# Kernel tuning notes

Measured on AMD Instinct MI355X. Metric: run time of the kernel, lower is better.

## Reference

```python
import jax, jax.numpy as jnp
import numpy as np

RESERVOIR_SIZE = 2048
EMBED = 768
N_FRAMES = 256
NUM_CLASSES = 1000
BATCH = 128
SPARSITY = 0.05
SPECTRAL_RADIUS = 0.8


def _init_reservoir(key):
    k1, k2 = jax.random.split(key)
    w = jax.random.normal(k1, (RESERVOIR_SIZE, RESERVOIR_SIZE), dtype=jnp.float32)
    mask = (jax.random.uniform(k2, (RESERVOIR_SIZE, RESERVOIR_SIZE)) < SPARSITY).astype(jnp.float32)
    r = w * mask
    # rescale so spectral radius == SPECTRAL_RADIUS (matches torch eigvals-based init)
    eig = np.linalg.eigvals(np.asarray(r))
    max_abs = np.abs(eig).max()
    return r * (SPECTRAL_RADIUS / jnp.float32(max_abs))


def setup_inputs() -> dict:
    key = jax.random.key(0)
    kx, kr, kin, kout = jax.random.split(key, 4)
    x = jax.random.normal(kx, (BATCH, N_FRAMES, EMBED), dtype=jnp.float32)
    reservoir = _init_reservoir(kr)
    W_in = jax.random.normal(kin, (RESERVOIR_SIZE, EMBED), dtype=jnp.float32) * 0.1
    W_out = jax.random.normal(kout, (NUM_CLASSES, RESERVOIR_SIZE), dtype=jnp.float32) * 0.02
    b_out = jnp.zeros((NUM_CLASSES,), dtype=jnp.float32)
    return {"x": x, "reservoir": reservoir, "W_in": W_in, "W_out": W_out, "b_out": b_out}


def reference(x, reservoir, W_in, W_out, b_out):
    # x: [B, T, E]. Precompute input projections for all frames in one GEMM:
    # u[t] = x[:, t] @ W_in.T  -> [T, B, R]
    u = jnp.einsum("bte,re->tbr", x, W_in)
    state0 = jnp.zeros((x.shape[0], reservoir.shape[0]), dtype=x.dtype)

    def step(state, u_t):
        new_state = jnp.tanh(state @ reservoir.T + u_t)
        return new_state, None

    state, _ = jax.lax.scan(step, state0, u)
    # linear head (dropout is identity in eval mode)
    logits = state @ W_out.T + b_out
    return logits
```

## Files before the change

### kernel.cpp

```cpp
#include <hip/hip_runtime.h>
#include <stdint.h>
#include <stddef.h>

#define BATCH 128
#define NFRAMES 256
#define EMBED 768
#define RES 2048
#define NCLS 1000
#define NWG 256

typedef __attribute__((ext_vector_type(8))) short bf16x8;
typedef __attribute__((ext_vector_type(4))) float f32x4;
typedef unsigned short u16;

__device__ inline u16 f2bf(float f) {
    union { float f; unsigned u; } v; v.f = f;
    unsigned r = v.u + 0x7FFFu + ((v.u >> 16) & 1u);
    return (u16)(r >> 16);
}
__device__ inline float bf2f(u16 h) {
    union { unsigned u; float f; } v; v.u = ((unsigned)h) << 16;
    return v.f;
}
__device__ inline float tanh_fast(float x) {
    float z = __builtin_amdgcn_exp2f(x * 2.885390081777927f);
    return 1.f - 2.f * __builtin_amdgcn_rcpf(z + 1.f);
}

__global__ __launch_bounds__(256) void cvt_kernel(const float* __restrict__ in,
                                                  u16* __restrict__ out, int n4) {
    int i = blockIdx.x * blockDim.x + threadIdx.x;
    int stride = gridDim.x * blockDim.x;
    for (; i < n4; i += stride) {
        float4 v = ((const float4*)in)[i];
        ushort4 o;
        o.x = f2bf(v.x); o.y = f2bf(v.y); o.z = f2bf(v.z); o.w = f2bf(v.w);
        ((ushort4*)out)[i] = o;
    }
}

__global__ __launch_bounds__(256) void proj_kernel(const u16* __restrict__ xb,
                                                   const u16* __restrict__ win,
                                                   u16* __restrict__ u) {
    int lane = threadIdx.x & 63;
    int w = threadIdx.x >> 6;
    int wm = w >> 1, wn = w & 1;
    int m0 = blockIdx.x * 128 + wm * 64;
    int n0 = blockIdx.y * 128 + wn * 64;
    int lr = lane & 15;
    int lk = (lane >> 4) * 8;

    f32x4 acc[4][4];
#pragma unroll
    for (int i = 0; i < 4; i++)
#pragma unroll
        for (int j = 0; j < 4; j++) acc[i][j] = (f32x4)0.f;

    for (int kk = 0; kk < EMBED; kk += 32) {
        bf16x8 a[4], b[4];
#pragma unroll
        for (int i = 0; i < 4; i++)
            a[i] = *(const bf16x8*)(xb + (size_t)(m0 + i * 16 + lr) * EMBED + kk + lk);
#pragma unroll
        for (int j = 0; j < 4; j++)
            b[j] = *(const bf16x8*)(win + (size_t)(n0 + j * 16 + lr) * EMBED + kk + lk);
#pragma unroll
        for (int i = 0; i < 4; i++)
#pragma unroll
            for (int j = 0; j < 4; j++)
                acc[i][j] = __builtin_amdgcn_mfma_f32_16x16x32_bf16(a[i], b[j], acc[i][j], 0, 0, 0);
    }

    int rowbase = (lane >> 4) * 4;
#pragma unroll
    for (int i = 0; i < 4; i++) {
#pragma unroll
        for (int j = 0; j < 4; j++) {
#pragma unroll
            for (int q = 0; q < 4; q++) {
                int m = m0 + i * 16 + rowbase + q;
                int n = n0 + j * 16 + lr;
                int bb = m >> 8, tt = m & 255;
                u[((size_t)tt * BATCH + bb) * RES + n] = f2bf(acc[i][j][q]);
            }
        }
    }
}

__global__ __launch_bounds__(512, 1) void recur_kernel(const u16* __restrict__ res,
                                                       u16* __restrict__ u,
                                                       const u16* __restrict__ s0,
                                                       unsigned* __restrict__ flags) {
    __shared__ float part[8][16][66];
    const int lane = threadIdx.x & 63;
    const int w = threadIdx.x >> 6;
    const int rowgrp = (int)(blockIdx.x & 7);
    const int colblk = (int)(blockIdx.x >> 3);
    const int m0 = rowgrp * 16;
    const int n0 = colblk * 64;
    const int lr = lane & 15;
    const int lk = (lane >> 4) * 8;
    const int rb = (lane >> 4) * 4;
    const int kbase = w * 256;
    unsigned* myflag = flags + rowgrp * 32 + colblk;
    const unsigned* pollflag = flags + rowgrp * 32 + (lane & 31);

    bf16x8 bfr[4][8];
#pragma unroll
    for (int jf = 0; jf < 4; jf++)
#pragma unroll
        for (int kk = 0; kk < 8; kk++) {
            const u16* bp = res + (size_t)(n0 + jf * 16 + lr) * RES + kbase + kk * 32 + lk;
            asm volatile("global_load_dwordx4 %0, %1, off"
                         : "=v"(bfr[jf][kk]) : "v"(bp));
        }
    asm volatile("s_waitcnt vmcnt(0)" ::: "memory");

    const int er = threadIdx.x >> 5;
    const int ec = (threadIdx.x & 31) * 2;
    const size_t gidx = (size_t)(m0 + er) * RES + n0 + ec;

    for (int t = 0; t < NFRAMES; t++) {
        const u16* sin = (t == 0) ? s0 : u + (size_t)(t - 1) * BATCH * RES;
        u16* sout = u + (size_t)t * BATCH * RES;
        const u16* abase = sin + (size_t)(m0 + lr) * RES + kbase + lk;

        unsigned uv = *(const unsigned*)(sout + gidx);

        bf16x8 a[8];
#pragma unroll
        for (int kk = 0; kk < 8; kk++)
            asm volatile("global_load_dwordx4 %0, %1, off"
                         : "=v"(a[kk]) : "v"(abase + kk * 32));

        f32x4 acc[4];
#pragma unroll
        for (int jf = 0; jf < 4; jf++) acc[jf] = (f32x4)0.f;

        asm volatile("s_waitcnt vmcnt(4)" ::: "memory");
        __builtin_amdgcn_sched_barrier(0);
#pragma unroll
        for (int kk = 0; kk < 4; kk++)
#pragma unroll
            for (int jf = 0; jf < 4; jf++)
                acc[jf] = __builtin_amdgcn_mfma_f32_16x16x32_bf16(a[kk], bfr[jf][kk], acc[jf], 0, 0, 0);
        asm volatile("s_waitcnt vmcnt(0)" ::: "memory");
        __builtin_amdgcn_sched_barrier(0);
#pragma unroll
        for (int kk = 4; kk < 8; kk++)
#pragma unroll
            for (int jf = 0; jf < 4; jf++)
                acc[jf] = __builtin_amdgcn_mfma_f32_16x16x32_bf16(a[kk], bfr[jf][kk], acc[jf], 0, 0, 0);

#pragma unroll
        for (int jf = 0; jf < 4; jf++)
#pragma unroll
            for (int q = 0; q < 4; q++)
                part[w][rb + q][jf * 16 + lr] = acc[jf][q];
        __syncthreads();

        float sx = 0.f, sy = 0.f;
#pragma unroll
        for (int ww = 0; ww < 8; ww++) {
            float2 v = *(const float2*)&part[ww][er][ec];
            sx += v.x; sy += v.y;
        }
        float v0 = tanh_fast(sx + bf2f((u16)(uv & 0xFFFF)));
        float v1 = tanh_fast(sy + bf2f((u16)(uv >> 16)));
        unsigned pk = (unsigned)f2bf(v0) | ((unsigned)f2bf(v1) << 16);
        asm volatile("global_store_dword %0, %1, off sc0 sc1"
                     :: "v"(sout + gidx), "v"(pk) : "memory");

        asm volatile("s_waitcnt vmcnt(0)" ::: "memory");
        __syncthreads();
        if (t != NFRAMES - 1) {
            unsigned stamp = (unsigned)(t + 1);
            if (w == 0) {
                if (lane == 0)
                    asm volatile("global_store_dword %0, %1, off sc0 sc1"
                                 :: "v"(myflag), "v"(stamp) : "memory");
                unsigned f;
                do {
                    asm volatile("global_load_dword %0, %1, off sc0 sc1\n\ts_waitcnt vmcnt(0)"
                                 : "=v"(f) : "v"(pollflag) : "memory");
                    if (__all((int)(f >= stamp))) break;
                    __builtin_amdgcn_s_sleep(2);
                } while (1);
            }
            __syncthreads();
        }
    }
}

__global__ __launch_bounds__(512) void head_kernel(const u16* __restrict__ sin,
                                                   const u16* __restrict__ wout,
                                                   const float* __restrict__ bias,
                                                   float* __restrict__ out) {
    __shared__ float part[8][32][33];
    int lane = threadIdx.x & 63;
    int w = threadIdx.x >> 6;
    int m0 = blockIdx.x * 32;
    int n0 = blockIdx.y * 32;
    int k0 = w * 256;
    int lr = lane & 15;
    int lk = (lane >> 4) * 8;

    f32x4 acc[2][2];
#pragma unroll
    for (int i = 0; i < 2; i++)
#pragma unroll
        for (int j = 0; j < 2; j++) acc[i][j] = (f32x4)0.f;

    for (int kk = k0; kk < k0 + 256; kk += 32) {
        bf16x8 a[2], b[2];
#pragma unroll
        for (int i = 0; i < 2; i++)
            a[i] = *(const bf16x8*)(sin + (size_t)(m0 + i * 16 + lr) * RES + kk + lk);
#pragma unroll
        for (int j = 0; j < 2; j++) {
            int row = n0 + j * 16 + lr;
            if (row > NCLS - 1) row = NCLS - 1;
            b[j] = *(const bf16x8*)(wout + (size_t)row * RES + kk + lk);
        }
#pragma unroll
        for (int i = 0; i < 2; i++)
#pragma unroll
            for (int j = 0; j < 2; j++)
                acc[i][j] = __builtin_amdgcn_mfma_f32_16x16x32_bf16(a[i], b[j], acc[i][j], 0, 0, 0);
    }

    int rowbase = (lane >> 4) * 4;
#pragma unroll
    for (int i = 0; i < 2; i++)
#pragma unroll
        for (int j = 0; j < 2; j++)
#pragma unroll
            for (int q = 0; q < 4; q++)
                part[w][i * 16 + rowbase + q][j * 16 + lr] = acc[i][j][q];

    __syncthreads();

    for (int idx = threadIdx.x; idx < 1024; idx += 512) {
        int r = idx >> 5, c = idx & 31;
        float s = 0.f;
#pragma unroll
        for (int ww = 0; ww < 8; ww++) s += part[ww][r][c];
        int cg = n0 + c;
        if (cg < NCLS)
            out[(size_t)(m0 + r) * NCLS + cg] = s + bias[cg];
    }
}

extern "C" void kernel_launch(void* const* d_in, const int* in_sizes, int n_in,
                              void* d_out, int out_size, void* d_ws, size_t ws_size,
                              hipStream_t stream) {
    const float* x_f    = (const float*)d_in[0];
    const float* res_f  = (const float*)d_in[1];
    const float* win_f  = (const float*)d_in[2];
    const float* wout_f = (const float*)d_in[3];
    const float* bias   = (const float*)d_in[4];
    float* out = (float*)d_out;

    char* ws = (char*)d_ws;
    size_t off = 0;
    auto alloc = [&](size_t bytes) -> void* {
        void* p = ws + off;
        off += (bytes + 255) & ~(size_t)255;
        return p;
    };
    u16* res_b  = (u16*)alloc((size_t)RES * RES * 2);
    u16* win_b  = (u16*)alloc((size_t)RES * EMBED * 2);
    u16* wout_b = (u16*)alloc((size_t)NCLS * RES * 2);
    u16* x_b    = (u16*)alloc((size_t)BATCH * NFRAMES * EMBED * 2);
    u16* u      = (u16*)alloc((size_t)NFRAMES * BATCH * RES * 2);
    u16* s0     = (u16*)alloc((size_t)BATCH * RES * 2);
    unsigned* flags = (unsigned*)alloc(1024);

    cvt_kernel<<<dim3(1024), dim3(256), 0, stream>>>(res_f, res_b, RES * RES / 4);
    cvt_kernel<<<dim3(512), dim3(256), 0, stream>>>(win_f, win_b, RES * EMBED / 4);
    cvt_kernel<<<dim3(512), dim3(256), 0, stream>>>(wout_f, wout_b, NCLS * RES / 4);
    cvt_kernel<<<dim3(2048), dim3(256), 0, stream>>>(x_f, x_b, BATCH * NFRAMES * EMBED / 4);

    hipMemsetAsync(s0, 0, (size_t)BATCH * RES * 2, stream);
    hipMemsetAsync(flags, 0, 1024, stream);

    proj_kernel<<<dim3(256, 16), dim3(256), 0, stream>>>(x_b, win_b, u);

    void* args[] = { (void*)&res_b, (void*)&u, (void*)&s0, (void*)&flags };
    hipLaunchCooperativeKernel((const void*)recur_kernel, dim3(NWG), dim3(512),
                               args, 0, stream);

    const u16* sfin = u + (size_t)(NFRAMES - 1) * BATCH * RES;
    head_kernel<<<dim3(4, 32), dim3(512), 0, stream>>>(sfin, wout_b, bias, out);
}
```

Measured before the change: 1.405 ms.

## Halve recurrent workgroups, each handling two row groups with staggered flag sync

```diff
diff --git a/kernel.cpp b/kernel.cpp
--- a/kernel.cpp
+++ b/kernel.cpp
@@ -7,7 +7,7 @@
 #define EMBED 768
 #define RES 2048
 #define NCLS 1000
-#define NWG 256
+#define NWG 128
 
 typedef __attribute__((ext_vector_type(8))) short bf16x8;
 typedef __attribute__((ext_vector_type(4))) float f32x4;
@@ -25,6 +25,15 @@
 __device__ inline float tanh_fast(float x) {
     float z = __builtin_amdgcn_exp2f(x * 2.885390081777927f);
     return 1.f - 2.f * __builtin_amdgcn_rcpf(z + 1.f);
+}
+__device__ inline void poll32(const unsigned* pf, unsigned stamp) {
+    unsigned f;
+    do {
+        asm volatile("global_load_dword %0, %1, off sc0 sc1\n\ts_waitcnt vmcnt(0)"
+                     : "=v"(f) : "v"(pf) : "memory");
+        if (__all((int)(f >= stamp))) break;
+        __builtin_amdgcn_s_sleep(2);
+    } while (1);
 }
 
 __global__ __launch_bounds__(256) void cvt_kernel(const float* __restrict__ in,
@@ -94,16 +103,19 @@
     __shared__ float part[8][16][66];
     const int lane = threadIdx.x & 63;
     const int w = threadIdx.x >> 6;
-    const int rowgrp = (int)(blockIdx.x & 7);
-    const int colblk = (int)(blockIdx.x >> 3);
-    const int m0 = rowgrp * 16;
-    const int n0 = colblk * 64;
+    const int c = (int)(blockIdx.x & 31);
+    const int p = (int)(blockIdx.x >> 5);
+    const int g0 = p, g1 = p + 4;
+    const int m0a = g0 * 16, m0b = g1 * 16;
+    const int n0 = c * 64;
     const int lr = lane & 15;
     const int lk = (lane >> 4) * 8;
     const int rb = (lane >> 4) * 4;
     const int kbase = w * 256;
-    unsigned* myflag = flags + rowgrp * 32 + colblk;
-    const unsigned* pollflag = flags + rowgrp * 32 + (lane & 31);
+    unsigned* myflag0 = flags + g0 * 32 + c;
+    unsigned* myflag1 = flags + g1 * 32 + c;
+    const unsigned* pollflag0 = flags + g0 * 32 + (lane & 31);
+    const unsigned* pollflag1 = flags + g1 * 32 + (lane & 31);
 
     bf16x8 bfr[4][8];
 #pragma unroll
@@ -118,39 +130,89 @@
 
     const int er = threadIdx.x >> 5;
     const int ec = (threadIdx.x & 31) * 2;
-    const size_t gidx = (size_t)(m0 + er) * RES + n0 + ec;
+    const size_t gcol = (size_t)er * RES + n0 + ec;
+    const size_t gidx0 = (size_t)m0a * RES + gcol;
+    const size_t gidx1 = (size_t)m0b * RES + gcol;
 
     for (int t = 0; t < NFRAMES; t++) {
         const u16* sin = (t == 0) ? s0 : u + (size_t)(t - 1) * BATCH * RES;
         u16* sout = u + (size_t)t * BATCH * RES;
-        const u16* abase = sin + (size_t)(m0 + lr) * RES + kbase + lk;
-
-        unsigned uv = *(const unsigned*)(sout + gidx);
-
-        bf16x8 a[8];
+        const unsigned stamp = (unsigned)(t + 1);
+
+        if (t > 0) {
+            if (w == 0) poll32(pollflag0, (unsigned)t);
+            __syncthreads();
+        }
+        unsigned uv0 = *(const unsigned*)(sout + gidx0);
+
+        const u16* abase0 = sin + (size_t)(m0a + lr) * RES + kbase + lk;
+        bf16x8 a0[8];
 #pragma unroll
         for (int kk = 0; kk < 8; kk++)
             asm volatile("global_load_dwordx4 %0, %1, off"
-                         : "=v"(a[kk]) : "v"(abase + kk * 32));
+                         : "=v"(a0[kk]) : "v"(abase0 + kk * 32));
 
         f32x4 acc[4];
 #pragma unroll
         for (int jf = 0; jf < 4; jf++) acc[jf] = (f32x4)0.f;
-
         asm volatile("s_waitcnt vmcnt(4)" ::: "memory");
         __builtin_amdgcn_sched_barrier(0);
 #pragma unroll
         for (int kk = 0; kk < 4; kk++)
 #pragma unroll
             for (int jf = 0; jf < 4; jf++)
-                acc[jf] = __builtin_amdgcn_mfma_f32_16x16x32_bf16(a[kk], bfr[jf][kk], acc[jf], 0, 0, 0);
+                acc[jf] = __builtin_amdgcn_mfma_f32_16x16x32_bf16(a0[kk], bfr[jf][kk], acc[jf], 0, 0, 0);
         asm volatile("s_waitcnt vmcnt(0)" ::: "memory");
         __builtin_amdgcn_sched_barrier(0);
 #pragma unroll
         for (int kk = 4; kk < 8; kk++)
 #pragma unroll
             for (int jf = 0; jf < 4; jf++)
-                acc[jf] = __builtin_amdgcn_mfma_f32_16x16x32_bf16(a[kk], bfr[jf][kk], acc[jf], 0, 0, 0);
+                acc[jf] = __builtin_amdgcn_mfma_f32_16x16x32_bf16(a0[kk], bfr[jf][kk], acc[jf], 0, 0, 0);
+
+#pragma unroll
+        for (int jf = 0; jf < 4; jf++)
+#pragma unroll
+            for (int q = 0; q < 4; q++)
+                part[w][rb + q][jf * 16 + lr] = acc[jf][q];
+        if (t > 0 && w == 0) poll32(pollflag1, (unsigned)t);
+        __syncthreads();
+
+        unsigned uv1 = *(const unsigned*)(sout + gidx1);
+        const u16* abase1 = sin + (size_t)(m0b + lr) * RES + kbase + lk;
+        bf16x8 a1[8];
+#pragma unroll
+        for (int kk = 0; kk < 8; kk++)
+            asm volatile("global_load_dwordx4 %0, %1, off"
+                         : "=v"(a1[kk]) : "v"(abase1 + kk * 32));
+
+        {
+            float sx = 0.f, sy = 0.f;
+#pragma unroll
+            for (int ww = 0; ww < 8; ww++) {
+                float2 v = *(const float2*)&part[ww][er][ec];
+                sx += v.x; sy += v.y;
+            }
+            float v0 = tanh_fast(sx + bf2f((u16)(uv0 & 0xFFFF)));
+            float v1 = tanh_fast(sy + bf2f((u16)(uv0 >> 16)));
+            unsigned pk = (unsigned)f2bf(v0) | ((unsigned)f2bf(v1) << 16);
+            asm volatile("global_store_dword %0, %1, off sc0 sc1"
+                         :: "v"(sout + gidx0), "v"(pk) : "memory");
+        }
+        asm volatile("s_waitcnt vmcnt(0)" ::: "memory");
+        __builtin_amdgcn_sched_barrier(0);
+        __syncthreads();
+        if (t != NFRAMES - 1 && threadIdx.x == 0)
+            asm volatile("global_store_dword %0, %1, off sc0 sc1"
+                         :: "v"(myflag0), "v"(stamp) : "memory");
+
+#pragma unroll
+        for (int jf = 0; jf < 4; jf++) acc[jf] = (f32x4)0.f;
+#pragma unroll
+        for (int kk = 0; kk < 8; kk++)
+#pragma unroll
+            for (int jf = 0; jf < 4; jf++)
+                acc[jf] = __builtin_amdgcn_mfma_f32_16x16x32_bf16(a1[kk], bfr[jf][kk], acc[jf], 0, 0, 0);
 
 #pragma unroll
         for (int jf = 0; jf < 4; jf++)
@@ -159,36 +221,24 @@
                 part[w][rb + q][jf * 16 + lr] = acc[jf][q];
         __syncthreads();
 
-        float sx = 0.f, sy = 0.f;
-#pragma unroll
-        for (int ww = 0; ww < 8; ww++) {
-            float2 v = *(const float2*)&part[ww][er][ec];
-            sx += v.x; sy += v.y;
-        }
-        float v0 = tanh_fast(sx + bf2f((u16)(uv & 0xFFFF)));
-        float v1 = tanh_fast(sy + bf2f((u16)(uv >> 16)));
-        unsigned pk = (unsigned)f2bf(v0) | ((unsigned)f2bf(v1) << 16);
-        asm volatile("global_store_dword %0, %1, off sc0 sc1"
-                     :: "v"(sout + gidx), "v"(pk) : "memory");
-
+        {
+            float sx = 0.f, sy = 0.f;
+#pragma unroll
+            for (int ww = 0; ww < 8; ww++) {
+                float2 v = *(const float2*)&part[ww][er][ec];
+                sx += v.x; sy += v.y;
+            }
+            float v0 = tanh_fast(sx + bf2f((u16)(uv1 & 0xFFFF)));
+            float v1 = tanh_fast(sy + bf2f((u16)(uv1 >> 16)));
+            unsigned pk = (unsigned)f2bf(v0) | ((unsigned)f2bf(v1) << 16);
+            asm volatile("global_store_dword %0, %1, off sc0 sc1"
+                         :: "v"(sout + gidx1), "v"(pk) : "memory");
+        }
         asm volatile("s_waitcnt vmcnt(0)" ::: "memory");
         __syncthreads();
-        if (t != NFRAMES - 1) {
-            unsigned stamp = (unsigned)(t + 1);
-            if (w == 0) {
-                if (lane == 0)
-                    asm volatile("global_store_dword %0, %1, off sc0 sc1"
-                                 :: "v"(myflag), "v"(stamp) : "memory");
-                unsigned f;
-                do {
-                    asm volatile("global_load_dword %0, %1, off sc0 sc1\n\ts_waitcnt vmcnt(0)"
-                                 : "=v"(f) : "v"(pollflag) : "memory");
-                    if (__all((int)(f >= stamp))) break;
-                    __builtin_amdgcn_s_sleep(2);
-                } while (1);
-            }
-            __syncthreads();
-        }
+        if (t != NFRAMES - 1 && threadIdx.x == 0)
+            asm volatile("global_store_dword %0, %1, off sc0 sc1"
+                         :: "v"(myflag1), "v"(stamp) : "memory");
     }
 }
 
```

After: 2.001 ms. +42.4%, slower.
